# Performance work log

Measured on AMD Instinct MI355X. Metric: run time of the kernel, lower is better.

Reference implementation:

```python
import jax, jax.numpy as jnp
import numpy as np

B, S, HID = 2, 2048, 4096
H, HKV, DH = 32, 8, 128
G = H // HKV  # num_key_value_groups
WIN = 1024   # sliding window
THETA = 10000.0


def setup_inputs() -> dict:
    key = jax.random.key(0)
    ks = jax.random.split(key, 6)
    sc = 0.02
    hidden_states = jax.random.normal(ks[0], (B, S, HID), jnp.float32)
    q_proj_w = jax.random.normal(ks[1], (HID, HID), jnp.float32) * sc
    k_proj_w = jax.random.normal(ks[2], (HKV * DH, HID), jnp.float32) * sc
    v_proj_w = jax.random.normal(ks[3], (HKV * DH, HID), jnp.float32) * sc
    o_proj_w = jax.random.normal(ks[4], (HID, HID), jnp.float32) * sc
    i = jnp.arange(S)[:, None]
    j = jnp.arange(S)[None, :]
    allowed = (i >= j) & ((i - j) < WIN)
    attention_mask = jnp.where(allowed, 0.0, -1e9).astype(jnp.float32)
    attention_mask = jnp.broadcast_to(attention_mask[None, None], (B, 1, S, S))
    position_ids = jnp.broadcast_to(jnp.arange(S, dtype=jnp.int64)[None], (B, S))
    return {
        "hidden_states": hidden_states,
        "q_proj_w": q_proj_w,
        "k_proj_w": k_proj_w,
        "v_proj_w": v_proj_w,
        "o_proj_w": o_proj_w,
        "attention_mask": attention_mask,
        "position_ids": position_ids,
    }


def _rope_cos_sin(position_ids):
    # inv_freq: [DH/2]
    inv_freq = 1.0 / (THETA ** (jnp.arange(0, DH, 2, dtype=jnp.float32) / DH))
    # angles: [B, S, DH/2]
    ang = position_ids.astype(jnp.float32)[..., None] * inv_freq
    emb = jnp.concatenate([ang, ang], axis=-1)  # [B, S, DH]
    return jnp.cos(emb), jnp.sin(emb)


def _rotate_half(x):
    x1, x2 = x[..., : DH // 2], x[..., DH // 2:]
    return jnp.concatenate([-x2, x1], axis=-1)


def reference(hidden_states, q_proj_w, k_proj_w, v_proj_w, o_proj_w,
              attention_mask, position_ids):
    b, s, _ = hidden_states.shape
    # projections -> [b, heads, s, dh]
    q = (hidden_states @ q_proj_w.T).reshape(b, s, H, DH).transpose(0, 2, 1, 3)
    k = (hidden_states @ k_proj_w.T).reshape(b, s, HKV, DH).transpose(0, 2, 1, 3)
    v = (hidden_states @ v_proj_w.T).reshape(b, s, HKV, DH).transpose(0, 2, 1, 3)
    # RoPE (cos/sin indexed by position_ids, unsqueeze at head dim)
    cos, sin = _rope_cos_sin(position_ids)      # [b, s, dh]
    cos = cos[:, None]                           # [b, 1, s, dh]
    sin = sin[:, None]
    q = q * cos + _rotate_half(q) * sin
    k = k * cos + _rotate_half(k) * sin
    # GQA: group queries over kv heads (repeat_kv-style, no materialized repeat)
    qg = q.reshape(b, HKV, G, s, DH)
    scale = 1.0 / jnp.sqrt(jnp.asarray(DH, jnp.float32))
    scores = jnp.einsum("bkgqd,bksd->bkgqs", qg, k) * scale  # [b,hkv,g,s,s]
    scores = scores + attention_mask[:, :, None]              # [b,1,1,s,s] bc
    attn = jax.nn.softmax(scores.astype(jnp.float32), axis=-1).astype(q.dtype)
    ctx = jnp.einsum("bkgqs,bksd->bkgqd", attn, v)            # [b,hkv,g,s,dh]
    ctx = ctx.reshape(b, H, s, DH).transpose(0, 2, 1, 3).reshape(b, s, HID)
    return ctx @ o_proj_w.T
```

## Files before the change

kernel.cpp:

```cpp
#include <hip/hip_runtime.h>

typedef __attribute__((ext_vector_type(8))) short bf16x8;
typedef __attribute__((ext_vector_type(4))) float f32x4;

#define DEV static __device__ __forceinline__

DEV ushort f2bf(float f){
  unsigned u = __float_as_uint(f);
  u += 0x7FFFu + ((u >> 16) & 1u);
  return (ushort)(u >> 16);
}
DEV float bf2f(ushort b){ return __uint_as_float(((unsigned)b) << 16); }

DEV void gload_lds16(const void* g, void* l){
  __builtin_amdgcn_global_load_lds((const __attribute__((address_space(1))) void*)g,
                                   (__attribute__((address_space(3))) void*)l, 16, 0, 0);
}

DEV unsigned halfword(int4 v, int e){
  unsigned w;
  switch (e >> 1) { case 0: w = (unsigned)v.x; break;
                    case 1: w = (unsigned)v.y; break;
                    case 2: w = (unsigned)v.z; break;
                    default: w = (unsigned)v.w; }
  return (e & 1) ? (w >> 16) : (w & 0xFFFFu);
}

__global__ void castk(const float* __restrict__ src, ushort* __restrict__ dst, int n4){
  int stride = gridDim.x * blockDim.x;
  for (int i = blockIdx.x * blockDim.x + threadIdx.x; i < n4; i += stride){
    float4 v = reinterpret_cast<const float4*>(src)[i];
    ushort4 o;
    o.x = f2bf(v.x); o.y = f2bf(v.y); o.z = f2bf(v.z); o.w = f2bf(v.w);
    reinterpret_cast<ushort4*>(dst)[i] = o;
  }
}

template<typename OutT>
__global__ void gemm_bt(const ushort* __restrict__ A, const ushort* __restrict__ Bm,
                        OutT* __restrict__ C, int M, int N, int K){
  __shared__ alignas(16) ushort As[128*32];
  __shared__ alignas(16) ushort Bs[128*32];
  const int nTn = N >> 7;
  const int nwg = (M >> 7) * nTn;
  const int cpx = nwg >> 3;
  int bid = blockIdx.x;
  int wg  = (bid & 7) * cpx + (bid >> 3);
  int tm = wg / nTn, tn = wg % nTn;
  int t = threadIdx.x, w = t >> 6, l = t & 63;
  int lr = l & 15, lg = l >> 4;
  int wr = w >> 1, wc = w & 1;

  f32x4 acc[4][4] = {};
  const ushort* Abase = A + (size_t)(tm*128)*K;
  const ushort* Bbase = Bm + (size_t)(tn*128)*K;

  for (int kt = 0; kt < K; kt += 32){
    __syncthreads();
    #pragma unroll
    for (int i = 0; i < 2; i++){
      int off = (w*2+i)*1024 + l*16;
      int row = off >> 6, cole = (off & 63) >> 1;
      gload_lds16(Abase + (size_t)row*K + kt + cole, (char*)As + (w*2+i)*1024);
    }
    #pragma unroll
    for (int i = 0; i < 2; i++){
      int off = (w*2+i)*1024 + l*16;
      int row = off >> 6, cole = (off & 63) >> 1;
      gload_lds16(Bbase + (size_t)row*K + kt + cole, (char*)Bs + (w*2+i)*1024);
    }
    __syncthreads();
    bf16x8 af[4], bfr[4];
    #pragma unroll
    for (int mi = 0; mi < 4; mi++)
      af[mi] = *reinterpret_cast<const bf16x8*>(&As[(wr*64 + mi*16 + lr)*32 + lg*8]);
    #pragma unroll
    for (int ni = 0; ni < 4; ni++)
      bfr[ni] = *reinterpret_cast<const bf16x8*>(&Bs[(wc*64 + ni*16 + lr)*32 + lg*8]);
    #pragma unroll
    for (int mi = 0; mi < 4; mi++)
      #pragma unroll
      for (int ni = 0; ni < 4; ni++)
        acc[mi][ni] = __builtin_amdgcn_mfma_f32_16x16x32_bf16(af[mi], bfr[ni], acc[mi][ni], 0, 0, 0);
  }

  #pragma unroll
  for (int mi = 0; mi < 4; mi++)
    #pragma unroll
    for (int ni = 0; ni < 4; ni++)
      #pragma unroll
      for (int r = 0; r < 4; r++){
        int row = tm*128 + wr*64 + mi*16 + lg*4 + r;
        int col = tn*128 + wc*64 + ni*16 + lr;
        float v = acc[mi][ni][r];
        if constexpr (sizeof(OutT) == 2) C[(size_t)row*N + col] = (OutT)f2bf(v);
        else                             C[(size_t)row*N + col] = v;
      }
}

__global__ __launch_bounds__(256) void rope_kernel(ushort* __restrict__ qkv){
  int bs = blockIdx.x;
  int s  = bs & 2047;
  int d  = threadIdx.x & 63, hg = threadIdx.x >> 6;
  float inv = __builtin_amdgcn_exp2f(-(float)d * (13.287712379549449f / 64.0f));
  float ang = (float)s * inv;
  float c = cosf(ang), sn = sinf(ang);
  ushort* row = qkv + (size_t)bs * 6144;
  for (int hh = hg; hh < 40; hh += 4){
    ushort* p = row + hh*128;
    float x1 = bf2f(p[d]), x2 = bf2f(p[d+64]);
    p[d]    = f2bf(x1*c - x2*sn);
    p[d+64] = f2bf(x2*c + x1*sn);
  }
}

__global__ __launch_bounds__(256) void attn_kernel(const ushort* __restrict__ qkv,
                                                   ushort* __restrict__ ctx){
  constexpr int RS = 6144;
  constexpr int KSb = 272, VTSb = 144, PSb = 144;
  __shared__ alignas(16) char Ks [64*KSb];
  __shared__ alignas(16) char VTs[128*VTSb];
  __shared__ alignas(16) char Ps [4*16*PSb];
  int t = threadIdx.x, w = t >> 6, l = t & 63;
  int lr = l & 15, lg = l >> 4;
  int bid = blockIdx.x;
  int qb = bid & 31, hq = (bid >> 5) & 31, b = bid >> 10;
  int kvh = hq >> 2;
  const ushort* Qb = qkv + (size_t)(b*2048)*RS + hq*128;
  const ushort* Kb = qkv + (size_t)(b*2048)*RS + 4096 + kvh*128;
  const ushort* Vb = qkv + (size_t)(b*2048)*RS + 5120 + kvh*128;
  int i0 = qb*64, i0w = i0 + w*16;
  char* Pw = Ps + w*16*PSb;

  bf16x8 qf[4];
  {
    const ushort* qr = Qb + (size_t)(i0w + lr)*RS + lg*8;
    #pragma unroll
    for (int c = 0; c < 4; c++) qf[c] = *reinterpret_cast<const bf16x8*>(qr + c*32);
  }
  f32x4 acco[8] = {};
  float mrow[4] = {-1e30f,-1e30f,-1e30f,-1e30f};
  float lsum[4] = {0.f,0.f,0.f,0.f};
  const float SCALE = 0.08838834764831845f;
  const float L2E   = 1.4426950408889634f;
  int t0 = qb >= 16 ? qb - 16 : 0;

  for (int tt = t0; tt <= qb; ++tt){
    int j0 = tt*64;
    __syncthreads();
    #pragma unroll
    for (int i = 0; i < 4; i++){
      int c = t + 256*i;
      int row = c >> 4, cole = (c & 15)*8;
      int4 v = *reinterpret_cast<const int4*>(Kb + (size_t)(j0+row)*RS + cole);
      *reinterpret_cast<int4*>(&Ks[row*KSb + cole*2]) = v;
    }
    #pragma unroll
    for (int i = 0; i < 2; i++){
      int u = t + 256*i;
      int cp = u & 15, rp = u >> 4;
      const ushort* vr = Vb + (size_t)(j0 + 2*rp)*RS + cp*8;
      int4 vlo = *reinterpret_cast<const int4*>(vr);
      int4 vhi = *reinterpret_cast<const int4*>(vr + RS);
      #pragma unroll
      for (int e = 0; e < 8; e++){
        unsigned pk = halfword(vlo, e) | (halfword(vhi, e) << 16);
        int dh = cp*8 + e;
        *reinterpret_cast<unsigned*>(&VTs[dh*VTSb + ((rp*4) ^ ((cp & 7) << 4))]) = pk;
      }
    }
    __syncthreads();

    f32x4 accs[4] = {};
    #pragma unroll
    for (int c = 0; c < 4; c++)
      #pragma unroll
      for (int n = 0; n < 4; n++){
        bf16x8 kb = *reinterpret_cast<const bf16x8*>(&Ks[(n*16+lr)*KSb + (c*32+lg*8)*2]);
        accs[n] = __builtin_amdgcn_mfma_f32_16x16x32_bf16(qf[c], kb, accs[n], 0, 0, 0);
      }

    const bool needMask = (tt == qb) || (tt == qb - 16);
    float sc[4][4];
    #pragma unroll
    for (int n = 0; n < 4; n++)
      #pragma unroll
      for (int r = 0; r < 4; r++){
        float v = accs[n][r] * SCALE;
        if (needMask){
          int ii = i0w + lg*4 + r;
          int jj = j0 + n*16 + lr;
          if (jj > ii || ii - jj >= 1024) v = -3e38f;
        }
        sc[n][r] = v;
      }
    float corr[4];
    #pragma unroll
    for (int r = 0; r < 4; r++){
      float tmv = fmaxf(fmaxf(sc[0][r], sc[1][r]), fmaxf(sc[2][r], sc[3][r]));
      #pragma unroll
      for (int d2 = 1; d2 < 16; d2 <<= 1) tmv = fmaxf(tmv, __shfl_xor(tmv, d2));
      float mn = fmaxf(mrow[r], tmv);
      corr[r] = __builtin_amdgcn_exp2f((mrow[r] - mn) * L2E);
      mrow[r] = mn;
    }
    float pv[4][4], ps[4] = {0.f,0.f,0.f,0.f};
    #pragma unroll
    for (int n = 0; n < 4; n++)
      #pragma unroll
      for (int r = 0; r < 4; r++){
        float p = __builtin_amdgcn_exp2f((sc[n][r] - mrow[r]) * L2E);
        pv[n][r] = p; ps[r] += p;
      }
    #pragma unroll
    for (int r = 0; r < 4; r++){
      float s2 = ps[r];
      #pragma unroll
      for (int d2 = 1; d2 < 16; d2 <<= 1) s2 += __shfl_xor(s2, d2);
      lsum[r] = lsum[r]*corr[r] + s2;
    }
    #pragma unroll
    for (int n = 0; n < 8; n++)
      #pragma unroll
      for (int r = 0; r < 4; r++) acco[n][r] *= corr[r];

    #pragma unroll
    for (int n = 0; n < 4; n++)
      #pragma unroll
      for (int r = 0; r < 4; r++)
        *reinterpret_cast<ushort*>(&Pw[(lg*4+r)*PSb + (n*16+lr)*2]) = f2bf(pv[n][r]);
    #pragma unroll
    for (int cc = 0; cc < 2; cc++){
      bf16x8 pa = *reinterpret_cast<const bf16x8*>(&Pw[lr*PSb + (cc*32+lg*8)*2]);
      #pragma unroll
      for (int n = 0; n < 8; n++){
        int dh = n*16 + lr;
        int kvb = (cc*64 + lg*16) ^ (((dh >> 3) & 7) << 4);
        bf16x8 vb = *reinterpret_cast<const bf16x8*>(&VTs[dh*VTSb + kvb]);
        acco[n] = __builtin_amdgcn_mfma_f32_16x16x32_bf16(pa, vb, acco[n], 0, 0, 0);
      }
    }
  }

  float rinv[4];
  #pragma unroll
  for (int r = 0; r < 4; r++) rinv[r] = 1.0f / lsum[r];
  #pragma unroll
  for (int n = 0; n < 8; n++)
    #pragma unroll
    for (int r = 0; r < 4; r++){
      int i = i0w + lg*4 + r;
      ctx[(size_t)(b*2048 + i)*4096 + hq*128 + n*16 + lr] = f2bf(acco[n][r]*rinv[r]);
    }
}

extern "C" void kernel_launch(void* const* d_in, const int* in_sizes, int n_in,
                              void* d_out, int out_size, void* d_ws, size_t ws_size,
                              hipStream_t stream) {
  const float* hs = (const float*)d_in[0];
  const float* qw = (const float*)d_in[1];
  const float* kw = (const float*)d_in[2];
  const float* vw = (const float*)d_in[3];
  const float* ow = (const float*)d_in[4];
  float* out = (float*)d_out;

  ushort* ws    = (ushort*)d_ws;
  ushort* hs_bf = ws;
  ushort* wqkv  = ws + 16777216;
  ushort* wo    = wqkv + 25165824;
  ushort* qkvo  = wo + 16777216;
  ushort* ctx   = hs_bf;

  castk<<<2048, 256, 0, stream>>>(hs, hs_bf, 4194304);
  castk<<<2048, 256, 0, stream>>>(qw, wqkv,            4194304);
  castk<<< 512, 256, 0, stream>>>(kw, wqkv + 16777216, 1048576);
  castk<<< 512, 256, 0, stream>>>(vw, wqkv + 20971520, 1048576);
  castk<<<2048, 256, 0, stream>>>(ow, wo, 4194304);

  gemm_bt<ushort><<<1536, 256, 0, stream>>>(hs_bf, wqkv, qkvo, 4096, 6144, 4096);
  rope_kernel<<<4096, 256, 0, stream>>>(qkvo);
  attn_kernel<<<2048, 256, 0, stream>>>(qkvo, ctx);
  gemm_bt<float><<<1024, 256, 0, stream>>>(ctx, wo, out, 4096, 4096, 4096);
}
```

Baseline: 881.4 us.

## Replace GEMM with 256x256-tile, 4-stage LDS-pipelined MFMA kernel

Measured after the change: 890.1 us. About the same (+1.0%).

```diff
diff --git a/kernel.cpp b/kernel.cpp
--- a/kernel.cpp
+++ b/kernel.cpp
@@ -37,61 +37,107 @@
 }
 
 template<typename OutT>
-__global__ void gemm_bt(const ushort* __restrict__ A, const ushort* __restrict__ Bm,
-                        OutT* __restrict__ C, int M, int N, int K){
-  __shared__ alignas(16) ushort As[128*32];
-  __shared__ alignas(16) ushort Bs[128*32];
-  const int nTn = N >> 7;
-  const int nwg = (M >> 7) * nTn;
+__global__ __launch_bounds__(512, 2) void gemm256(const ushort* __restrict__ A,
+                                                  const ushort* __restrict__ Bm,
+                                                  OutT* __restrict__ C, int M, int N, int K){
+  __shared__ alignas(16) ushort As[4*8192];
+  __shared__ alignas(16) ushort Bs[4*8192];
+  const int nTn = N >> 8;
+  const int nwg = (M >> 8) * nTn;
   const int cpx = nwg >> 3;
   int bid = blockIdx.x;
   int wg  = (bid & 7) * cpx + (bid >> 3);
   int tm = wg / nTn, tn = wg % nTn;
-  int t = threadIdx.x, w = t >> 6, l = t & 63;
+  int u = threadIdx.x, w = u >> 6, l = u & 63;
   int lr = l & 15, lg = l >> 4;
-  int wr = w >> 1, wc = w & 1;
-
-  f32x4 acc[4][4] = {};
-  const ushort* Abase = A + (size_t)(tm*128)*K;
-  const ushort* Bbase = Bm + (size_t)(tn*128)*K;
-
-  for (int kt = 0; kt < K; kt += 32){
-    __syncthreads();
-    #pragma unroll
-    for (int i = 0; i < 2; i++){
-      int off = (w*2+i)*1024 + l*16;
-      int row = off >> 6, cole = (off & 63) >> 1;
-      gload_lds16(Abase + (size_t)row*K + kt + cole, (char*)As + (w*2+i)*1024);
-    }
-    #pragma unroll
-    for (int i = 0; i < 2; i++){
-      int off = (w*2+i)*1024 + l*16;
-      int row = off >> 6, cole = (off & 63) >> 1;
-      gload_lds16(Bbase + (size_t)row*K + kt + cole, (char*)Bs + (w*2+i)*1024);
-    }
-    __syncthreads();
-    bf16x8 af[4], bfr[4];
-    #pragma unroll
-    for (int mi = 0; mi < 4; mi++)
-      af[mi] = *reinterpret_cast<const bf16x8*>(&As[(wr*64 + mi*16 + lr)*32 + lg*8]);
+  int wm = w >> 2, wn = w & 3;
+  const ushort* Abase = A + (size_t)(tm*256)*K;
+  const ushort* Bbase = Bm + (size_t)(tn*256)*K;
+  const int NT = K >> 5;
+
+  f32x4 acc[8][4] = {};
+
+  auto stage = [&](int t){
+    int s = t & 3;
+    #pragma unroll
+    for (int l2 = 0; l2 < 2; l2++){
+      int c = l2*512 + u;
+      int row = c >> 2, kc = (c & 3)*8;
+      gload_lds16(Abase + (size_t)row*K + t*32 + kc, &As[s*8192 + c*8]);
+    }
+    #pragma unroll
+    for (int l2 = 0; l2 < 2; l2++){
+      int c = l2*512 + u;
+      int row = c >> 2, kc = (c & 3)*8;
+      gload_lds16(Bbase + (size_t)row*K + t*32 + kc, &Bs[s*8192 + c*8]);
+    }
+  };
+
+  stage(0); stage(1); stage(2);
+  asm volatile("s_waitcnt vmcnt(8)" ::: "memory");
+  __builtin_amdgcn_s_barrier();
+  __builtin_amdgcn_sched_barrier(0);
+
+  for (int t = 0; t < NT; ++t){
+    int st = t & 3;
+    const ushort* ApS = &As[st*8192 + (wm*128 + lr)*32 + lg*8];
+    const ushort* BpS = &Bs[st*8192 + (wn*64  + lr)*32 + lg*8];
+
+    bf16x8 b0 = *reinterpret_cast<const bf16x8*>(BpS);
+    bf16x8 b1 = *reinterpret_cast<const bf16x8*>(BpS + 16*32);
+    bf16x8 b2 = *reinterpret_cast<const bf16x8*>(BpS + 32*32);
+    bf16x8 b3 = *reinterpret_cast<const bf16x8*>(BpS + 48*32);
+    bf16x8 a0 = *reinterpret_cast<const bf16x8*>(ApS);
+    bf16x8 a1 = *reinterpret_cast<const bf16x8*>(ApS + 16*32);
+    bf16x8 a2 = *reinterpret_cast<const bf16x8*>(ApS + 32*32);
+    bf16x8 a3 = *reinterpret_cast<const bf16x8*>(ApS + 48*32);
+
+    if (t + 3 < NT) stage(t + 3);
+
+    __builtin_amdgcn_s_setprio(1);
+    #pragma unroll
+    for (int ni = 0; ni < 4; ni++){
+      bf16x8 bf = ni==0?b0: ni==1?b1: ni==2?b2: b3;
+      acc[0][ni] = __builtin_amdgcn_mfma_f32_16x16x32_bf16(a0, bf, acc[0][ni], 0, 0, 0);
+      acc[1][ni] = __builtin_amdgcn_mfma_f32_16x16x32_bf16(a1, bf, acc[1][ni], 0, 0, 0);
+      acc[2][ni] = __builtin_amdgcn_mfma_f32_16x16x32_bf16(a2, bf, acc[2][ni], 0, 0, 0);
+      acc[3][ni] = __builtin_amdgcn_mfma_f32_16x16x32_bf16(a3, bf, acc[3][ni], 0, 0, 0);
+    }
+    __builtin_amdgcn_s_setprio(0);
+
+    bf16x8 a4 = *reinterpret_cast<const bf16x8*>(ApS + 64*32);
+    bf16x8 a5 = *reinterpret_cast<const bf16x8*>(ApS + 80*32);
+    bf16x8 a6 = *reinterpret_cast<const bf16x8*>(ApS + 96*32);
+    bf16x8 a7 = *reinterpret_cast<const bf16x8*>(ApS + 112*32);
+
+    __builtin_amdgcn_s_setprio(1);
+    #pragma unroll
+    for (int ni = 0; ni < 4; ni++){
+      bf16x8 bf = ni==0?b0: ni==1?b1: ni==2?b2: b3;
+      acc[4][ni] = __builtin_amdgcn_mfma_f32_16x16x32_bf16(a4, bf, acc[4][ni], 0, 0, 0);
+      acc[5][ni] = __builtin_amdgcn_mfma_f32_16x16x32_bf16(a5, bf, acc[5][ni], 0, 0, 0);
+      acc[6][ni] = __builtin_amdgcn_mfma_f32_16x16x32_bf16(a6, bf, acc[6][ni], 0, 0, 0);
+      acc[7][ni] = __builtin_amdgcn_mfma_f32_16x16x32_bf16(a7, bf, acc[7][ni], 0, 0, 0);
+    }
+    __builtin_amdgcn_s_setprio(0);
+
+    if (t < NT-3)       asm volatile("s_waitcnt vmcnt(8)" ::: "memory");
+    else if (t == NT-3) asm volatile("s_waitcnt vmcnt(4)" ::: "memory");
+    else if (t == NT-2) asm volatile("s_waitcnt vmcnt(0)" ::: "memory");
+    if (t < NT-1){
+      __builtin_amdgcn_s_barrier();
+      __builtin_amdgcn_sched_barrier(0);
+    }
+  }
+
+  #pragma unroll
+  for (int mi = 0; mi < 8; mi++)
     #pragma unroll
     for (int ni = 0; ni < 4; ni++)
-      bfr[ni] = *reinterpret_cast<const bf16x8*>(&Bs[(wc*64 + ni*16 + lr)*32 + lg*8]);
-    #pragma unroll
-    for (int mi = 0; mi < 4; mi++)
-      #pragma unroll
-      for (int ni = 0; ni < 4; ni++)
-        acc[mi][ni] = __builtin_amdgcn_mfma_f32_16x16x32_bf16(af[mi], bfr[ni], acc[mi][ni], 0, 0, 0);
-  }
-
-  #pragma unroll
-  for (int mi = 0; mi < 4; mi++)
-    #pragma unroll
-    for (int ni = 0; ni < 4; ni++)
       #pragma unroll
       for (int r = 0; r < 4; r++){
-        int row = tm*128 + wr*64 + mi*16 + lg*4 + r;
-        int col = tn*128 + wc*64 + ni*16 + lr;
+        int row = tm*256 + wm*128 + mi*16 + lg*4 + r;
+        int col = tn*256 + wn*64  + ni*16 + lr;
         float v = acc[mi][ni][r];
         if constexpr (sizeof(OutT) == 2) C[(size_t)row*N + col] = (OutT)f2bf(v);
         else                             C[(size_t)row*N + col] = v;
@@ -277,8 +323,8 @@
   castk<<< 512, 256, 0, stream>>>(vw, wqkv + 20971520, 1048576);
   castk<<<2048, 256, 0, stream>>>(ow, wo, 4194304);
 
-  gemm_bt<ushort><<<1536, 256, 0, stream>>>(hs_bf, wqkv, qkvo, 4096, 6144, 4096);
+  gemm256<ushort><<<384, 512, 0, stream>>>(hs_bf, wqkv, qkvo, 4096, 6144, 4096);
   rope_kernel<<<4096, 256, 0, stream>>>(qkvo);
   attn_kernel<<<2048, 256, 0, stream>>>(qkvo, ctx);
-  gemm_bt<float><<<1024, 256, 0, stream>>>(ctx, wo, out, 4096, 4096, 4096);
-}
+  gemm256<float><<<256, 512, 0, stream>>>(ctx, wo, out, 4096, 4096, 4096);
+}
```
